# Optimization experiments

Measured on AMD Instinct MI355X. Metric: run time of the kernel, lower is better.

Reference implementation:

```python
import jax, jax.numpy as jnp
import numpy as np

B, S, D, H = 4, 2048, 1024, 16
HD = D // H  # head dim = 64

def setup_inputs() -> dict:
    key = jax.random.key(0)
    ks = jax.random.split(key, 11)
    s = 1.0 / np.sqrt(D)
    return {
        "q": jax.random.normal(ks[0], (B, S, D), jnp.float32),
        "k": jax.random.normal(ks[1], (B, S, D), jnp.float32),
        "v": jax.random.normal(ks[2], (B, S, D), jnp.float32),
        "Wq": jax.random.normal(ks[3], (D, D), jnp.float32) * s,
        "bq": jnp.zeros((D,), jnp.float32),
        "Wk": jax.random.normal(ks[4], (D, D), jnp.float32) * s,
        "bk": jnp.zeros((D,), jnp.float32),
        "Wv": jax.random.normal(ks[5], (D, D), jnp.float32) * s,
        "bv": jnp.zeros((D,), jnp.float32),
        "Wo": jax.random.normal(ks[6], (D, D), jnp.float32) * s,
        "bo": jnp.zeros((D,), jnp.float32),
    }

def reference(q, k, v, Wq, bq, Wk, bk, Wv, bv, Wo, bo):
    b, n, _ = q.shape
    # QKV projections, split heads -> [b, s, h, hd]
    qh = (q @ Wq + bq).reshape(b, n, H, HD)
    kh = (k @ Wk + bk).reshape(b, k.shape[1], H, HD)
    vh = (v @ Wv + bv).reshape(b, v.shape[1], H, HD)
    scale = 1.0 / np.sqrt(HD)
    scores = jnp.einsum('blhe,bshe->bhls', qh, kh)  # [b,h,l,s]
    attn = jax.nn.softmax(scale * scores, axis=-1)  # dropout is identity in eval
    out = jnp.einsum('bhls,bshd->blhd', attn, vh)   # [b,l,h,hd]
    out = out.reshape(b, n, H * HD)
    return out @ Wo + bo
```

## Files before the change

### kernel.cpp

```cpp
#include <hip/hip_runtime.h>
#include <cstdint>

#define DEV __device__ __forceinline__

typedef __attribute__((ext_vector_type(8))) __bf16 bf16x8;
typedef __attribute__((ext_vector_type(2))) unsigned u32x2;
typedef __attribute__((ext_vector_type(4))) float f32x4;

DEV unsigned short f2b(float f) {
  unsigned u = __builtin_bit_cast(unsigned, f);
  u += 0x7fffu + ((u >> 16) & 1u);
  return (unsigned short)(u >> 16);
}

DEV unsigned pkrn(float f0, float f1) {
  unsigned a0 = __builtin_bit_cast(unsigned, f0) + 0x8000u;
  unsigned a1 = __builtin_bit_cast(unsigned, f1) + 0x8000u;
#if __has_builtin(__builtin_amdgcn_perm)
  return __builtin_amdgcn_perm(a1, a0, 0x07060302u);
#else
  return (a0 >> 16) | (a1 & 0xffff0000u);
#endif
}

DEV float exp2_fast(float x) {
#if __has_builtin(__builtin_amdgcn_exp2f)
  return __builtin_amdgcn_exp2f(x);
#else
  return __expf(x * 0.6931471805599453f);
#endif
}

DEV void gload_lds16(const unsigned short* g, unsigned short* l) {
  __builtin_amdgcn_global_load_lds(
      (const __attribute__((address_space(1))) void*)g,
      (__attribute__((address_space(3))) void*)l, 16, 0, 0);
}

__global__ __launch_bounds__(256) void cvt3_kernel(const float* __restrict__ q,
                                                   const float* __restrict__ k,
                                                   const float* __restrict__ v,
                                                   unsigned short* __restrict__ dst) {
  int z = blockIdx.y;
  const float* src = (z == 0) ? q : (z == 1) ? k : v;
  unsigned short* d = dst + (size_t)z * 8192 * 1024;
  int i = blockIdx.x * 256 + threadIdx.x;
  const float4* s4 = (const float4*)src;
  float4 a = s4[2 * i], b = s4[2 * i + 1];
  uint4 o;
  o.x = (unsigned)f2b(a.x) | ((unsigned)f2b(a.y) << 16);
  o.y = (unsigned)f2b(a.z) | ((unsigned)f2b(a.w) << 16);
  o.z = (unsigned)f2b(b.x) | ((unsigned)f2b(b.y) << 16);
  o.w = (unsigned)f2b(b.z) | ((unsigned)f2b(b.w) << 16);
  ((uint4*)d)[i] = o;
}

__global__ __launch_bounds__(256) void wtr4_kernel(const float* __restrict__ W0,
                                                   const float* __restrict__ W1,
                                                   const float* __restrict__ W2,
                                                   const float* __restrict__ W3,
                                                   unsigned short* __restrict__ WtBase) {
  int z = blockIdx.z;
  const float* W = (z == 0) ? W0 : (z == 1) ? W1 : (z == 2) ? W2 : W3;
  unsigned short* Wt = WtBase + (size_t)z * 1024 * 1024;
  __shared__ float t[64][65];
  int n0 = blockIdx.x * 64, k0 = blockIdx.y * 64;
  int tx = threadIdx.x & 63, ty = threadIdx.x >> 6;
  for (int i = ty; i < 64; i += 4)
    t[i][tx] = W[(size_t)(k0 + i) * 1024 + n0 + tx];
  __syncthreads();
  for (int i = ty; i < 64; i += 4)
    Wt[(size_t)(n0 + i) * 1024 + k0 + tx] = f2b(t[tx][i]);
}

struct GemmAcc {
  f32x4 acc[4][4];
};

DEV void gemm_core(const unsigned short* __restrict__ A,
                   const unsigned short* __restrict__ Bt,
                   unsigned short* Al, unsigned short* Bl,
                   int m0, int n0, int K, GemmAcc& R) {
  int tid = threadIdx.x, wv = tid >> 6, ln = tid & 63;
  int wr = wv >> 1, wc = wv & 1;
  for (int i = 0; i < 4; i++)
    for (int j = 0; j < 4; j++) R.acc[i][j] = (f32x4)0.f;
  int lr = ln >> 3, lc = (ln & 7) * 8;
  for (int kt = 0; kt < K; kt += 64) {
    __syncthreads();
    for (int o = 0; o < 4; ++o) {
      int op = wv * 4 + o;
      int row = op * 8 + lr;
      gload_lds16(A + (size_t)(m0 + row) * K + kt + lc, &Al[op * 512]);
    }
    for (int o = 0; o < 4; ++o) {
      int op = wv * 4 + o;
      int row = op * 8 + lr;
      gload_lds16(Bt + (size_t)(n0 + row) * K + kt + lc, &Bl[op * 512]);
    }
    __syncthreads();
    for (int kk = 0; kk < 2; ++kk) {
      bf16x8 af[4], bfr[4];
      int ko = kk * 32 + (ln >> 4) * 8;
      for (int i = 0; i < 4; ++i)
        af[i] = *(const bf16x8*)&Al[(wr * 64 + i * 16 + (ln & 15)) * 64 + ko];
      for (int j = 0; j < 4; ++j)
        bfr[j] = *(const bf16x8*)&Bl[(wc * 64 + j * 16 + (ln & 15)) * 64 + ko];
      for (int i = 0; i < 4; ++i)
        for (int j = 0; j < 4; ++j)
          R.acc[i][j] = __builtin_amdgcn_mfma_f32_16x16x32_bf16(af[i], bfr[j], R.acc[i][j], 0, 0, 0);
    }
  }
}

__global__ __launch_bounds__(256) void gemm_qkv(const unsigned short* __restrict__ Xbase,
                                                const unsigned short* __restrict__ Wbase,
                                                const float* __restrict__ bq,
                                                const float* __restrict__ bk,
                                                const float* __restrict__ bv,
                                                unsigned short* __restrict__ Obase,
                                                float qscale) {
  __shared__ unsigned short Al[128 * 64];
  __shared__ unsigned short Bl[128 * 64];
  int z = blockIdx.z;
  const size_t NX = (size_t)8192 * 1024, NW = (size_t)1024 * 1024;
  const unsigned short* A = Xbase + (size_t)z * NX;
  const unsigned short* Bt = Wbase + (size_t)z * NW;
  const float* bias = (z == 0) ? bq : (z == 1) ? bk : bv;
  unsigned short* outp = Obase + (size_t)z * NX;
  int m0 = blockIdx.y * 128, n0 = blockIdx.x * 128;
  GemmAcc R;
  gemm_core(A, Bt, Al, Bl, m0, n0, 1024, R);
  int ln = threadIdx.x & 63, wv = threadIdx.x >> 6;
  int wr = wv >> 1, wc = wv & 1;
  int g = ln >> 4, c = ln & 15;
  if (z < 2) {
    float oscale = (z == 0) ? qscale : 1.0f;
    for (int j = 0; j < 4; ++j) {
      int gn = n0 + wc * 64 + j * 16 + c;
      float bs = bias[gn];
      int h_ = gn >> 6, hd = gn & 63;
      for (int i = 0; i < 4; ++i) {
        int gm0 = m0 + wr * 64 + i * 16 + g * 4;
        for (int r = 0; r < 4; ++r) {
          float vv = (R.acc[i][j][r] + bs) * oscale;
          int gm = gm0 + r;
          int b_ = gm >> 11, s_ = gm & 2047;
          outp[(((size_t)(b_ * 16 + h_) * 2048 + s_) << 6) + hd] = f2b(vv);
        }
      }
    }
  } else {
    int mb = m0 + wr * 64;
    int b_ = mb >> 11, st = (mb & 2047) >> 6;
    for (int j = 0; j < 4; ++j) {
      int gn = n0 + wc * 64 + j * 16 + c;
      float bs = bias[gn];
      int h_ = gn >> 6, hd = gn & 63;
      unsigned short* vrow = outp + (((size_t)((b_ * 16 + h_) * 32 + st) * 64 + hd) << 6);
      for (int r = 0; r < 4; ++r) {
        u32x2 w;
        w.x = pkrn(R.acc[0][j][r] + bs, R.acc[1][j][r] + bs);
        w.y = pkrn(R.acc[2][j][r] + bs, R.acc[3][j][r] + bs);
        *(u32x2*)&vrow[(g * 4 + r) * 4] = w;
      }
    }
  }
}

__global__ __launch_bounds__(256) void gemm_out(const unsigned short* __restrict__ A,
                                                const unsigned short* __restrict__ Bt,
                                                const float* __restrict__ bias,
                                                float* __restrict__ outp) {
  __shared__ unsigned short Al[128 * 64];
  __shared__ unsigned short Bl[128 * 64];
  int m0 = blockIdx.y * 128, n0 = blockIdx.x * 128;
  GemmAcc R;
  gemm_core(A, Bt, Al, Bl, m0, n0, 1024, R);
  int ln = threadIdx.x & 63, wv = threadIdx.x >> 6;
  int wr = wv >> 1, wc = wv & 1;
  int g = ln >> 4, c = ln & 15;
  for (int j = 0; j < 4; ++j) {
    int gn = n0 + wc * 64 + j * 16 + c;
    float bs = bias[gn];
    for (int i = 0; i < 4; ++i) {
      int gm0 = m0 + wr * 64 + i * 16 + g * 4;
      for (int r = 0; r < 4; ++r)
        outp[(size_t)(gm0 + r) * 1024 + gn] = R.acc[i][j][r] + bs;
    }
  }
}

__global__ __launch_bounds__(256) void attn_kernel(const unsigned short* __restrict__ Qh,
                                                   const unsigned short* __restrict__ Kh,
                                                   const unsigned short* __restrict__ VtG,
                                                   unsigned short* __restrict__ AttnOut) {
  __shared__ unsigned short Kl[64 * 64];
  __shared__ unsigned short Vl[64 * 64];
  __shared__ unsigned short Pl[4 * 32 * 72];
  int tid = threadIdx.x, wv = tid >> 6, ln = tid & 63;
  int qt = blockIdx.x, bh = blockIdx.y;
  const unsigned short* Qb = Qh + (size_t)bh * 2048 * 64;
  const unsigned short* Kb = Kh + (size_t)bh * 2048 * 64;
  const unsigned short* Vb = VtG + (size_t)bh * 2048 * 64;
  int q0 = qt * 128 + wv * 32;
  int g = ln >> 4, c = ln & 15;
  int lr = ln >> 3, lb = ln & 7;
  bf16x8 aq[2][2];
  for (int mi = 0; mi < 2; ++mi)
    for (int kk = 0; kk < 2; ++kk)
      aq[mi][kk] = *(const bf16x8*)(Qb + (size_t)(q0 + mi * 16 + c) * 64 + kk * 32 + g * 8);
  f32x4 o[2][4], lrun[2];
  for (int mi = 0; mi < 2; ++mi) {
    lrun[mi] = (f32x4)0.f;
    for (int j = 0; j < 4; ++j) o[mi][j] = (f32x4)0.f;
  }
  unsigned short* pw = &Pl[wv * 32 * 72];
  for (int kt = 0; kt < 2048; kt += 64) {
    __syncthreads();
    for (int ot = 0; ot < 2; ++ot) {
      int rb = wv * 16 + ot * 8;
      gload_lds16(Kb + (size_t)(kt + rb + lr) * 64 + (lb ^ lr) * 8, &Kl[rb * 64]);
    }
    const unsigned short* vtb = Vb + (size_t)(kt >> 6) * 4096;
    for (int ot = 0; ot < 2; ++ot) {
      int rb = wv * 16 + ot * 8;
      gload_lds16(vtb + (size_t)(rb + lr) * 64 + (lb ^ lr) * 8, &Vl[rb * 64]);
    }
    __syncthreads();
    f32x4 s[2][4];
    for (int mi = 0; mi < 2; ++mi)
      for (int j = 0; j < 4; ++j) s[mi][j] = (f32x4)0.f;
    for (int kk = 0; kk < 2; ++kk) {
      bf16x8 bk[4];
      for (int j = 0; j < 4; ++j)
        bk[j] = *(const bf16x8*)&Kl[(j * 16 + c) * 64 + ((kk * 4 + g) ^ (c & 7)) * 8];
      for (int mi = 0; mi < 2; ++mi)
        for (int j = 0; j < 4; ++j)
          s[mi][j] = __builtin_amdgcn_mfma_f32_16x16x32_bf16(aq[mi][kk], bk[j], s[mi][j], 0, 0, 0);
    }
    for (int mi = 0; mi < 2; ++mi)
      for (int j = 0; j < 4; ++j)
        for (int r = 0; r < 4; ++r) {
          float p = exp2_fast(s[mi][j][r]);
          s[mi][j][r] = p;
          lrun[mi][r] += p;
        }
    for (int mi = 0; mi < 2; ++mi)
      for (int r = 0; r < 4; ++r) {
        u32x2 w;
        w.x = pkrn(s[mi][0][r], s[mi][1][r]);
        w.y = pkrn(s[mi][2][r], s[mi][3][r]);
        *(u32x2*)&pw[(mi * 16 + g * 4 + r) * 72 + c * 4] = w;
      }
    __threadfence_block();
    for (int kk = 0; kk < 2; ++kk) {
      int ko = kk * 32 + g * 8;
      bf16x8 ap[2], bv[4];
      for (int mi = 0; mi < 2; ++mi) ap[mi] = *(const bf16x8*)&pw[(mi * 16 + c) * 72 + ko];
      for (int j = 0; j < 4; ++j)
        bv[j] = *(const bf16x8*)&Vl[(j * 16 + c) * 64 + ((kk * 4 + g) ^ (c & 7)) * 8];
      for (int mi = 0; mi < 2; ++mi)
        for (int j = 0; j < 4; ++j)
          o[mi][j] = __builtin_amdgcn_mfma_f32_16x16x32_bf16(ap[mi], bv[j], o[mi][j], 0, 0, 0);
    }
  }
  int b_ = bh >> 4, h_ = bh & 15;
  for (int mi = 0; mi < 2; ++mi) {
    float linv[4];
    for (int r = 0; r < 4; ++r) {
      float l = lrun[mi][r];
      for (int d = 1; d < 16; d <<= 1) l += __shfl_xor(l, d);
      linv[r] = 1.f / l;
    }
    for (int j = 0; j < 4; ++j)
      for (int r = 0; r < 4; ++r) {
        int row = q0 + mi * 16 + g * 4 + r;
        int col = h_ * 64 + j * 16 + c;
        float val = o[mi][j][r] * linv[r];
        AttnOut[((size_t)b_ * 2048 + row) * 1024 + col] = f2b(val);
      }
  }
}

extern "C" void kernel_launch(void* const* d_in, const int* in_sizes, int n_in,
                              void* d_out, int out_size, void* d_ws, size_t ws_size,
                              hipStream_t stream) {
  const float* q  = (const float*)d_in[0];
  const float* k  = (const float*)d_in[1];
  const float* v  = (const float*)d_in[2];
  const float* Wq = (const float*)d_in[3];
  const float* bq = (const float*)d_in[4];
  const float* Wk = (const float*)d_in[5];
  const float* bk = (const float*)d_in[6];
  const float* Wv = (const float*)d_in[7];
  const float* bv = (const float*)d_in[8];
  const float* Wo = (const float*)d_in[9];
  const float* bo = (const float*)d_in[10];
  float* out = (float*)d_out;

  unsigned short* ws = (unsigned short*)d_ws;
  const size_t NX = (size_t)8192 * 1024;
  const size_t NW = (size_t)1024 * 1024;
  unsigned short* X   = ws;
  unsigned short* Wt  = X + 3 * NX;
  unsigned short* QKV = Wt + 4 * NW;
  unsigned short* Ao  = X;

  const float qscale = 0.125f * 1.4426950408889634f;

  cvt3_kernel<<<dim3(4096, 3), 256, 0, stream>>>(q, k, v, X);
  wtr4_kernel<<<dim3(16, 16, 4), 256, 0, stream>>>(Wq, Wk, Wv, Wo, Wt);
  gemm_qkv<<<dim3(8, 64, 3), 256, 0, stream>>>(X, Wt, bq, bk, bv, QKV, qscale);
  attn_kernel<<<dim3(16, 64), 256, 0, stream>>>(QKV, QKV + NX, QKV + 2 * NX, Ao);
  gemm_out<<<dim3(8, 64), 256, 0, stream>>>(Ao, Wt + 3 * NW, bo, out);
}
```

Baseline: 371.9 us.

## Double-buffer K tiles in LDS, read V directly from global, use hardware bf16 pack

The attention loop now prefetches the next K tile into a second LDS buffer while computing on the current one, cutting to one barrier per iteration. V tiles are no longer staged in LDS; each wave loads its V fragments straight from global memory (likely served from L2, since every wave reads the same tile). The probability pack uses the v_cvt_pk_bf16_f32 instruction instead of manual bit rounding, and launch bounds request 4 blocks per CU. The risks are global-load latency on V sitting right before the PV MFMAs, more register pressure, and a slight change in rounding behaviour.

```diff
diff --git a/kernel.cpp b/kernel.cpp
--- a/kernel.cpp
+++ b/kernel.cpp
@@ -21,6 +21,12 @@
 #else
   return (a0 >> 16) | (a1 & 0xffff0000u);
 #endif
+}
+
+DEV unsigned cvtpk(float lo, float hi) {
+  unsigned r;
+  asm("v_cvt_pk_bf16_f32 %0, %1, %2" : "=v"(r) : "v"(lo), "v"(hi));
+  return r;
 }
 
 DEV float exp2_fast(float x) {
@@ -191,12 +197,11 @@
   }
 }
 
-__global__ __launch_bounds__(256) void attn_kernel(const unsigned short* __restrict__ Qh,
-                                                   const unsigned short* __restrict__ Kh,
-                                                   const unsigned short* __restrict__ VtG,
-                                                   unsigned short* __restrict__ AttnOut) {
-  __shared__ unsigned short Kl[64 * 64];
-  __shared__ unsigned short Vl[64 * 64];
+__global__ __launch_bounds__(256, 4) void attn_kernel(const unsigned short* __restrict__ Qh,
+                                                      const unsigned short* __restrict__ Kh,
+                                                      const unsigned short* __restrict__ VtG,
+                                                      unsigned short* __restrict__ AttnOut) {
+  __shared__ unsigned short Kl[2][64 * 64];
   __shared__ unsigned short Pl[4 * 32 * 72];
   int tid = threadIdx.x, wv = tid >> 6, ln = tid & 63;
   int qt = blockIdx.x, bh = blockIdx.y;
@@ -216,25 +221,27 @@
     for (int j = 0; j < 4; ++j) o[mi][j] = (f32x4)0.f;
   }
   unsigned short* pw = &Pl[wv * 32 * 72];
-  for (int kt = 0; kt < 2048; kt += 64) {
-    __syncthreads();
-    for (int ot = 0; ot < 2; ++ot) {
-      int rb = wv * 16 + ot * 8;
-      gload_lds16(Kb + (size_t)(kt + rb + lr) * 64 + (lb ^ lr) * 8, &Kl[rb * 64]);
-    }
-    const unsigned short* vtb = Vb + (size_t)(kt >> 6) * 4096;
-    for (int ot = 0; ot < 2; ++ot) {
-      int rb = wv * 16 + ot * 8;
-      gload_lds16(vtb + (size_t)(rb + lr) * 64 + (lb ^ lr) * 8, &Vl[rb * 64]);
-    }
-    __syncthreads();
+  for (int ot = 0; ot < 2; ++ot) {
+    int rb = wv * 16 + ot * 8;
+    gload_lds16(Kb + (size_t)(rb + lr) * 64 + (lb ^ lr) * 8, &Kl[0][rb * 64]);
+  }
+  __syncthreads();
+  for (int t = 0; t < 32; ++t) {
+    int cur = t & 1;
+    if (t < 31) {
+      int kt2 = (t + 1) * 64;
+      for (int ot = 0; ot < 2; ++ot) {
+        int rb = wv * 16 + ot * 8;
+        gload_lds16(Kb + (size_t)(kt2 + rb + lr) * 64 + (lb ^ lr) * 8, &Kl[cur ^ 1][rb * 64]);
+      }
+    }
     f32x4 s[2][4];
     for (int mi = 0; mi < 2; ++mi)
       for (int j = 0; j < 4; ++j) s[mi][j] = (f32x4)0.f;
     for (int kk = 0; kk < 2; ++kk) {
       bf16x8 bk[4];
       for (int j = 0; j < 4; ++j)
-        bk[j] = *(const bf16x8*)&Kl[(j * 16 + c) * 64 + ((kk * 4 + g) ^ (c & 7)) * 8];
+        bk[j] = *(const bf16x8*)&Kl[cur][(j * 16 + c) * 64 + ((kk * 4 + g) ^ (c & 7)) * 8];
       for (int mi = 0; mi < 2; ++mi)
         for (int j = 0; j < 4; ++j)
           s[mi][j] = __builtin_amdgcn_mfma_f32_16x16x32_bf16(aq[mi][kk], bk[j], s[mi][j], 0, 0, 0);
@@ -249,21 +256,26 @@
     for (int mi = 0; mi < 2; ++mi)
       for (int r = 0; r < 4; ++r) {
         u32x2 w;
-        w.x = pkrn(s[mi][0][r], s[mi][1][r]);
-        w.y = pkrn(s[mi][2][r], s[mi][3][r]);
+        w.x = cvtpk(s[mi][0][r], s[mi][1][r]);
+        w.y = cvtpk(s[mi][2][r], s[mi][3][r]);
         *(u32x2*)&pw[(mi * 16 + g * 4 + r) * 72 + c * 4] = w;
       }
     __threadfence_block();
-    for (int kk = 0; kk < 2; ++kk) {
-      int ko = kk * 32 + g * 8;
-      bf16x8 ap[2], bv[4];
-      for (int mi = 0; mi < 2; ++mi) ap[mi] = *(const bf16x8*)&pw[(mi * 16 + c) * 72 + ko];
-      for (int j = 0; j < 4; ++j)
-        bv[j] = *(const bf16x8*)&Vl[(j * 16 + c) * 64 + ((kk * 4 + g) ^ (c & 7)) * 8];
-      for (int mi = 0; mi < 2; ++mi)
-        for (int j = 0; j < 4; ++j)
-          o[mi][j] = __builtin_amdgcn_mfma_f32_16x16x32_bf16(ap[mi], bv[j], o[mi][j], 0, 0, 0);
-    }
+    const unsigned short* vtb = Vb + ((size_t)t << 12);
+    bf16x8 bva[4], bvb[4], ap[2];
+    for (int j = 0; j < 4; ++j)
+      bva[j] = *(const bf16x8*)(vtb + (j * 16 + c) * 64 + g * 8);
+    for (int j = 0; j < 4; ++j)
+      bvb[j] = *(const bf16x8*)(vtb + (j * 16 + c) * 64 + 32 + g * 8);
+    for (int mi = 0; mi < 2; ++mi) ap[mi] = *(const bf16x8*)&pw[(mi * 16 + c) * 72 + g * 8];
+    for (int mi = 0; mi < 2; ++mi)
+      for (int j = 0; j < 4; ++j)
+        o[mi][j] = __builtin_amdgcn_mfma_f32_16x16x32_bf16(ap[mi], bva[j], o[mi][j], 0, 0, 0);
+    for (int mi = 0; mi < 2; ++mi) ap[mi] = *(const bf16x8*)&pw[(mi * 16 + c) * 72 + 32 + g * 8];
+    for (int mi = 0; mi < 2; ++mi)
+      for (int j = 0; j < 4; ++j)
+        o[mi][j] = __builtin_amdgcn_mfma_f32_16x16x32_bf16(ap[mi], bvb[j], o[mi][j], 0, 0, 0);
+    __syncthreads();
   }
   int b_ = bh >> 4, h_ = bh & 15;
   for (int mi = 0; mi < 2; ++mi) {
```

New measurement: 410.0 us. 10.2% more time.
